# Kernel optimization log

Hardware: AMD Instinct MI355X
Metric: run time of the kernel (lower is better)

The kernel has to match this reference:

```python
import jax, jax.numpy as jnp
import numpy as np
import math

NEG = -10000.0  # module uses -10000, not -inf


def setup_inputs() -> dict:
    key = jax.random.key(0)
    k1, k2, k3 = jax.random.split(key, 3)
    B, Sq, Sk, H, Hkv, D = 2, 2048, 2048, 16, 4, 64
    q = jax.random.normal(k1, (B, Sq, H, D), dtype=jnp.float32)
    kv = jax.random.normal(k2, (B, Sk, 2, Hkv, D), dtype=jnp.float32)
    key_padding_mask = jax.random.randint(k3, (B, Sk), 0, 2) > 0  # True = valid key
    return {"q": q, "kv": kv, "key_padding_mask": key_padding_mask}


def reference(q, kv, key_padding_mask):
    B, Sq, H, D = q.shape
    Sk, Hkv = kv.shape[1], kv.shape[3]
    if Hkv != H:
        # einops repeat '... hkv d -> ... (hkv g) d': each kv head repeated g times contiguously
        kv = jnp.repeat(kv, H // Hkv, axis=3)
    k, v = kv[:, :, 0], kv[:, :, 1]  # [B, Sk, H, D] each
    scale = 1.0 / math.sqrt(D)
    scores = jnp.einsum('bthd,bshd->bhts', q, k * scale)  # [B, H, Sq, Sk]
    # key padding: additive 0 where valid, -10000 where padded
    pad = jnp.where(key_padding_mask, 0.0, NEG).astype(scores.dtype)
    scores = scores + pad[:, None, None, :]
    # causal mask: cols > rows + Sk - Sq gets replaced (not added) with -10000
    rows = jnp.arange(Sq)[:, None]
    cols = jnp.arange(Sk)[None, :]
    causal_mask = cols > rows + (Sk - Sq)
    scores = jnp.where(causal_mask, NEG, scores)
    attention = jax.nn.softmax(scores, axis=-1).astype(v.dtype)
    # dropout p=0.0 -> identity
    output = jnp.einsum('bhts,bshd->bthd', attention, v)  # [B, Sq, H, D]
    return output
```

## Files before the change

### kernel.cpp

```cpp
#include <hip/hip_runtime.h>
#include <math.h>


typedef __bf16 bf16x4 __attribute__((ext_vector_type(4)));
typedef __bf16 bf16x8 __attribute__((ext_vector_type(8)));
typedef float floatx4 __attribute__((ext_vector_type(4)));

#define B_ 2
#define SQ 2048
#define SK 2048
#define H_ 16
#define HKV 4
#define D_ 64
#define QT 64
#define KT 64
#define PADLD 72
#define KVROW 512
#define NEGV (-10000.0f)
#define QSCL 0.18033688f
#define EBIAS 17.3123405f

__global__ __launch_bounds__(256, 4)
void attn_kernel(const float* __restrict__ q,
                 const float* __restrict__ kv,
                 const int* __restrict__ mask,
                 float* __restrict__ out)
{
    __shared__ alignas(16) __bf16 Kt[KT][PADLD];
    __shared__ alignas(16) __bf16 Vt[D_][PADLD];
    __shared__ alignas(16) __bf16 Pl[4][16][PADLD];
    __shared__ float fpart[4][64];
    __shared__ float fw[4][64];
    __shared__ int s_first;

    const int tid  = threadIdx.x;
    const int wave = tid >> 6;
    const int lane = tid & 63;
    const int col  = lane & 15;
    const int quad = lane >> 4;

    if (blockIdx.x < 32) {
        const int bh = (int)blockIdx.x;
        const int b = bh >> 4, h = bh & 15, hkv = h >> 2;
        if (tid == 0) s_first = SK;
        __syncthreads();
        int local = SK;
        for (int s = tid; s < SK; s += 256)
            if (mask[b * SK + s]) local = min(local, s);
        atomicMin(&s_first, local);
        __syncthreads();
        const int nfirst = s_first;
        if (nfirst == 0) return;

        const float* kvb = kv + (size_t)b * SK * KVROW + hkv * D_;
        const float* vvb = kvb + HKV * D_;
        {
            float a0=0,a1=0,a2=0,a3=0,a4=0,a5=0,a6=0,a7=0;
            const int s0 = wave * 512;
            for (int s = s0; s < s0 + 512; s += 8) {
                a0 += vvb[(size_t)(s+0)*KVROW + lane];
                a1 += vvb[(size_t)(s+1)*KVROW + lane];
                a2 += vvb[(size_t)(s+2)*KVROW + lane];
                a3 += vvb[(size_t)(s+3)*KVROW + lane];
                a4 += vvb[(size_t)(s+4)*KVROW + lane];
                a5 += vvb[(size_t)(s+5)*KVROW + lane];
                a6 += vvb[(size_t)(s+6)*KVROW + lane];
                a7 += vvb[(size_t)(s+7)*KVROW + lane];
            }
            fpart[wave][lane] = ((a0+a1)+(a2+a3)) + ((a4+a5)+(a6+a7));
        }
        __syncthreads();
        const float vtotal = fpart[0][lane] + fpart[1][lane]
                           + fpart[2][lane] + fpart[3][lane];

        for (int R = wave; R < nfirst; R += 4) {
            const float* qrow = q + (((size_t)b * SQ + R) * H_ + h) * D_;
            float mymax = -3.4e38f;
            for (int s = lane; s <= R; s += 64) {
                const float* kp = kvb + (size_t)s * KVROW;
                float dt = 0.f;
                for (int d = 0; d < D_; ++d) dt += qrow[d] * kp[d];
                mymax = fmaxf(mymax, dt * 0.125f + NEGV);
            }
#pragma unroll
            for (int off = 32; off >= 1; off >>= 1)
                mymax = fmaxf(mymax, __shfl_xor(mymax, off, 64));
            const float M = (R < SK - 1) ? fmaxf(mymax, NEGV) : mymax;
            float lsum = 0.f, oacc = 0.f, pref = 0.f;
            for (int s0 = 0; s0 <= R; s0 += 64) {
                int s = s0 + lane;
                float w = 0.f;
                if (s <= R) {
                    const float* kp = kvb + (size_t)s * KVROW;
                    float dt = 0.f;
                    for (int d = 0; d < D_; ++d) dt += qrow[d] * kp[d];
                    w = __expf(dt * 0.125f + NEGV - M);
                    lsum += w;
                }
                fw[wave][lane] = w;
                const int nk = (R - s0 + 1 < 64) ? (R - s0 + 1) : 64;
                for (int j = 0; j < nk; ++j) {
                    const float vj = vvb[(size_t)(s0 + j) * KVROW + lane];
                    oacc += fw[wave][j] * vj;
                    pref += vj;
                }
            }
#pragma unroll
            for (int off = 32; off >= 1; off >>= 1)
                lsum += __shfl_xor(lsum, off, 64);
            const float wn   = __expf(NEGV - M);
            const float ltot = lsum + wn * (float)(SK - 1 - R);
            out[(((size_t)b * SQ + R) * H_ + h) * D_ + lane] =
                (oacc + wn * (vtotal - pref)) / ltot;
        }
        return;
    }

    const int id = (int)blockIdx.x - 32;
    const int bh = id & 31;
    const int y  = id >> 5;
    const int kg = y >> 3, jj = y & 7;
    const int qt = (kg == 0) ? 31 - jj : (kg == 1) ? jj : (kg == 2) ? 23 - jj : 8 + jj;
    const int b = bh >> 4, h = bh & 15, hkv = h >> 2;
    const int q0 = qt * QT;
    const int qw = q0 + wave * 16;

    bf16x8 aq[2];
    {
        const int row = qw + col;
        const float* qp = q + (((size_t)b * SQ + row) * H_ + h) * D_ + quad * 8;
#pragma unroll
        for (int kc = 0; kc < 2; ++kc) {
            const float* p = qp + kc * 32;
#pragma unroll
            for (int j = 0; j < 8; ++j) aq[kc][j] = (__bf16)(p[j] * QSCL);
        }
    }

    bf16x8 vone;
#pragma unroll
    for (int j = 0; j < 8; ++j) vone[j] = (__bf16)1.0f;

    floatx4 o[4];
    floatx4 l_acc = (floatx4){0.f, 0.f, 0.f, 0.f};
#pragma unroll
    for (int dj = 0; dj < 4; ++dj) o[dj] = (floatx4){0.f, 0.f, 0.f, 0.f};

    const int kkey = tid >> 4;
    const int kd   = (tid & 15) * 4;
    const int vkey = (tid & 15) * 4;
    const int vd   = (tid >> 4) * 4;

    const float* kvb = kv + (size_t)b * SK * KVROW + hkv * D_;

    float4 kreg[4], vreg[4];
    int mreg = 0;

    auto prefetch = [&](int kt) {
        const float* kb = kvb + (size_t)kt * KT * KVROW;
#pragma unroll
        for (int i = 0; i < 4; ++i)
            kreg[i] = *(const float4*)(kb + (kkey + 16 * i) * KVROW + kd);
        const float* vb = kb + HKV * D_;
#pragma unroll
        for (int i = 0; i < 4; ++i)
            vreg[i] = *(const float4*)(vb + (vkey + i) * KVROW + vd);
        mreg = mask[b * SK + kt * KT + lane];
    };

    auto stage = [&]() {
#pragma unroll
        for (int i = 0; i < 4; ++i) {
            bf16x4 t = { (__bf16)kreg[i].x, (__bf16)kreg[i].y,
                         (__bf16)kreg[i].z, (__bf16)kreg[i].w };
            *(bf16x4*)&Kt[kkey + 16 * i][kd] = t;
        }
        const float* vf = (const float*)vreg;
#pragma unroll
        for (int j = 0; j < 4; ++j) {
            bf16x4 t = { (__bf16)vf[0*4+j], (__bf16)vf[1*4+j],
                         (__bf16)vf[2*4+j], (__bf16)vf[3*4+j] };
            *(bf16x4*)&Vt[vd + j][vkey] = t;
        }
    };

    const int nkt = qt + 1;
    prefetch(0);

    for (int kt = 0; kt < nkt; ++kt) {
        stage();
        const unsigned long long kept = __ballot(mreg != 0);
        __syncthreads();
        if (kt + 1 < nkt) prefetch(kt + 1);

        floatx4 c[4];
#pragma unroll
        for (int kj = 0; kj < 4; ++kj) {
            c[kj] = (floatx4){0.f, 0.f, 0.f, 0.f};
#pragma unroll
            for (int kc = 0; kc < 2; ++kc) {
                bf16x8 bk = *(const bf16x8*)&Kt[kj * 16 + col][kc * 32 + quad * 8];
                c[kj] = __builtin_amdgcn_mfma_f32_16x16x32_bf16(aq[kc], bk, c[kj], 0, 0, 0);
            }
        }
        const bool dg = (kt == qt);
        const int rowl = wave * 16 + quad * 4;
#pragma unroll
        for (int kj = 0; kj < 4; ++kj) {
            const int keyl = kj * 16 + col;
            const bool keep = (kept >> keyl) & 1ull;
#pragma unroll
            for (int r = 0; r < 4; ++r) {
                float p = __builtin_amdgcn_exp2f(c[kj][r] - EBIAS);
                if (!keep) p = 0.f;
                if (dg && keyl > rowl + r) p = 0.f;
                Pl[wave][quad * 4 + r][keyl] = (__bf16)p;
            }
        }
        bf16x8 ap[2];
#pragma unroll
        for (int kc = 0; kc < 2; ++kc)
            ap[kc] = *(const bf16x8*)&Pl[wave][col][kc * 32 + quad * 8];
#pragma unroll
        for (int kc = 0; kc < 2; ++kc)
            l_acc = __builtin_amdgcn_mfma_f32_16x16x32_bf16(ap[kc], vone, l_acc, 0, 0, 0);
#pragma unroll
        for (int dj = 0; dj < 4; ++dj)
#pragma unroll
            for (int kc = 0; kc < 2; ++kc) {
                bf16x8 bv = *(const bf16x8*)&Vt[dj * 16 + col][kc * 32 + quad * 8];
                o[dj] = __builtin_amdgcn_mfma_f32_16x16x32_bf16(ap[kc], bv, o[dj], 0, 0, 0);
            }
        __syncthreads();
    }

#pragma unroll
    for (int r = 0; r < 4; ++r) {
        const float l = l_acc[r];
        if (l > 0.f) {
            const float inv = 1.0f / l;
            const int row = qw + quad * 4 + r;
            float* op = out + (((size_t)b * SQ + row) * H_ + h) * D_ + col;
#pragma unroll
            for (int dj = 0; dj < 4; ++dj)
                op[dj * 16] = o[dj][r] * inv;
        }
    }
}

extern "C" void kernel_launch(void* const* d_in, const int* in_sizes, int n_in,
                              void* d_out, int out_size, void* d_ws, size_t ws_size,
                              hipStream_t stream) {
    const float* q   = (const float*)d_in[0];
    const float* kv  = (const float*)d_in[1];
    const int* mask  = (const int*)d_in[2];
    float* out       = (float*)d_out;
    attn_kernel<<<dim3(32 + 1024), 256, 0, stream>>>(q, kv, mask, out);
}
```

Before: 126.4 us.

## Double query tile to 128 rows per block with two MFMA row groups per wave

Each block now handles 128 query rows, with each wave computing two 16-row groups against every staged K/V tile. This halves the K/V global loads and shared-memory staging per query row, and the grid shrinks to 512 attention blocks. Shared buffers for the fallback path and the main path are overlaid in a union to limit LDS growth, and waves skip tiles lying entirely above the causal diagonal. In exchange it uses more registers (launch bounds lowered to 3), launches fewer blocks so there is less parallelism and coarser load balance, and drops the earlier interleaved tile ordering.

```diff
diff --git a/kernel.cpp b/kernel.cpp
--- a/kernel.cpp
+++ b/kernel.cpp
@@ -12,7 +12,7 @@
 #define H_ 16
 #define HKV 4
 #define D_ 64
-#define QT 64
+#define QT 128
 #define KT 64
 #define PADLD 72
 #define KVROW 512
@@ -20,18 +20,24 @@
 #define QSCL 0.18033688f
 #define EBIAS 17.3123405f
 
-__global__ __launch_bounds__(256, 4)
+__global__ __launch_bounds__(256, 3)
 void attn_kernel(const float* __restrict__ q,
                  const float* __restrict__ kv,
                  const int* __restrict__ mask,
                  float* __restrict__ out)
 {
-    __shared__ alignas(16) __bf16 Kt[KT][PADLD];
-    __shared__ alignas(16) __bf16 Vt[D_][PADLD];
-    __shared__ alignas(16) __bf16 Pl[4][16][PADLD];
-    __shared__ float fpart[4][64];
-    __shared__ float fw[4][64];
-    __shared__ int s_first;
+    __shared__ alignas(16) union {
+        struct {
+            __bf16 Kt[KT][PADLD];
+            __bf16 Vt[D_][PADLD];
+            __bf16 Pl[4][32][PADLD];
+        } m;
+        struct {
+            float fpart[4][64];
+            float fw[4][64];
+            int   s_first;
+        } f;
+    } sh;
 
     const int tid  = threadIdx.x;
     const int wave = tid >> 6;
@@ -42,14 +48,14 @@
     if (blockIdx.x < 32) {
         const int bh = (int)blockIdx.x;
         const int b = bh >> 4, h = bh & 15, hkv = h >> 2;
-        if (tid == 0) s_first = SK;
+        if (tid == 0) sh.f.s_first = SK;
         __syncthreads();
         int local = SK;
         for (int s = tid; s < SK; s += 256)
             if (mask[b * SK + s]) local = min(local, s);
-        atomicMin(&s_first, local);
-        __syncthreads();
-        const int nfirst = s_first;
+        atomicMin(&sh.f.s_first, local);
+        __syncthreads();
+        const int nfirst = sh.f.s_first;
         if (nfirst == 0) return;
 
         const float* kvb = kv + (size_t)b * SK * KVROW + hkv * D_;
@@ -67,11 +73,11 @@
                 a6 += vvb[(size_t)(s+6)*KVROW + lane];
                 a7 += vvb[(size_t)(s+7)*KVROW + lane];
             }
-            fpart[wave][lane] = ((a0+a1)+(a2+a3)) + ((a4+a5)+(a6+a7));
-        }
-        __syncthreads();
-        const float vtotal = fpart[0][lane] + fpart[1][lane]
-                           + fpart[2][lane] + fpart[3][lane];
+            sh.f.fpart[wave][lane] = ((a0+a1)+(a2+a3)) + ((a4+a5)+(a6+a7));
+        }
+        __syncthreads();
+        const float vtotal = sh.f.fpart[0][lane] + sh.f.fpart[1][lane]
+                           + sh.f.fpart[2][lane] + sh.f.fpart[3][lane];
 
         for (int R = wave; R < nfirst; R += 4) {
             const float* qrow = q + (((size_t)b * SQ + R) * H_ + h) * D_;
@@ -97,11 +103,11 @@
                     w = __expf(dt * 0.125f + NEGV - M);
                     lsum += w;
                 }
-                fw[wave][lane] = w;
+                sh.f.fw[wave][lane] = w;
                 const int nk = (R - s0 + 1 < 64) ? (R - s0 + 1) : 64;
                 for (int j = 0; j < nk; ++j) {
                     const float vj = vvb[(size_t)(s0 + j) * KVROW + lane];
-                    oacc += fw[wave][j] * vj;
+                    oacc += sh.f.fw[wave][j] * vj;
                     pref += vj;
                 }
             }
@@ -119,21 +125,21 @@
     const int id = (int)blockIdx.x - 32;
     const int bh = id & 31;
     const int y  = id >> 5;
-    const int kg = y >> 3, jj = y & 7;
-    const int qt = (kg == 0) ? 31 - jj : (kg == 1) ? jj : (kg == 2) ? 23 - jj : 8 + jj;
+    const int qt = 15 - y;
     const int b = bh >> 4, h = bh & 15, hkv = h >> 2;
     const int q0 = qt * QT;
-    const int qw = q0 + wave * 16;
-
-    bf16x8 aq[2];
-    {
-        const int row = qw + col;
+    const int qw = q0 + wave * 32;
+
+    bf16x8 aq[2][2];
+#pragma unroll
+    for (int g = 0; g < 2; ++g) {
+        const int row = qw + g * 16 + col;
         const float* qp = q + (((size_t)b * SQ + row) * H_ + h) * D_ + quad * 8;
 #pragma unroll
         for (int kc = 0; kc < 2; ++kc) {
             const float* p = qp + kc * 32;
 #pragma unroll
-            for (int j = 0; j < 8; ++j) aq[kc][j] = (__bf16)(p[j] * QSCL);
+            for (int j = 0; j < 8; ++j) aq[g][kc][j] = (__bf16)(p[j] * QSCL);
         }
     }
 
@@ -141,10 +147,14 @@
 #pragma unroll
     for (int j = 0; j < 8; ++j) vone[j] = (__bf16)1.0f;
 
-    floatx4 o[4];
-    floatx4 l_acc = (floatx4){0.f, 0.f, 0.f, 0.f};
-#pragma unroll
-    for (int dj = 0; dj < 4; ++dj) o[dj] = (floatx4){0.f, 0.f, 0.f, 0.f};
+    floatx4 o[2][4];
+    floatx4 l_acc[2];
+#pragma unroll
+    for (int g = 0; g < 2; ++g) {
+        l_acc[g] = (floatx4){0.f, 0.f, 0.f, 0.f};
+#pragma unroll
+        for (int dj = 0; dj < 4; ++dj) o[g][dj] = (floatx4){0.f, 0.f, 0.f, 0.f};
+    }
 
     const int kkey = tid >> 4;
     const int kd   = (tid & 15) * 4;
@@ -173,18 +183,18 @@
         for (int i = 0; i < 4; ++i) {
             bf16x4 t = { (__bf16)kreg[i].x, (__bf16)kreg[i].y,
                          (__bf16)kreg[i].z, (__bf16)kreg[i].w };
-            *(bf16x4*)&Kt[kkey + 16 * i][kd] = t;
+            *(bf16x4*)&sh.m.Kt[kkey + 16 * i][kd] = t;
         }
         const float* vf = (const float*)vreg;
 #pragma unroll
         for (int j = 0; j < 4; ++j) {
             bf16x4 t = { (__bf16)vf[0*4+j], (__bf16)vf[1*4+j],
                          (__bf16)vf[2*4+j], (__bf16)vf[3*4+j] };
-            *(bf16x4*)&Vt[vd + j][vkey] = t;
+            *(bf16x4*)&sh.m.Vt[vd + j][vkey] = t;
         }
     };
 
-    const int nkt = qt + 1;
+    const int nkt = 2 * (qt + 1);
     prefetch(0);
 
     for (int kt = 0; kt < nkt; ++kt) {
@@ -193,59 +203,77 @@
         __syncthreads();
         if (kt + 1 < nkt) prefetch(kt + 1);
 
-        floatx4 c[4];
-#pragma unroll
-        for (int kj = 0; kj < 4; ++kj) {
-            c[kj] = (floatx4){0.f, 0.f, 0.f, 0.f};
-#pragma unroll
-            for (int kc = 0; kc < 2; ++kc) {
-                bf16x8 bk = *(const bf16x8*)&Kt[kj * 16 + col][kc * 32 + quad * 8];
-                c[kj] = __builtin_amdgcn_mfma_f32_16x16x32_bf16(aq[kc], bk, c[kj], 0, 0, 0);
-            }
-        }
-        const bool dg = (kt == qt);
-        const int rowl = wave * 16 + quad * 4;
-#pragma unroll
-        for (int kj = 0; kj < 4; ++kj) {
-            const int keyl = kj * 16 + col;
-            const bool keep = (kept >> keyl) & 1ull;
-#pragma unroll
-            for (int r = 0; r < 4; ++r) {
-                float p = __builtin_amdgcn_exp2f(c[kj][r] - EBIAS);
-                if (!keep) p = 0.f;
-                if (dg && keyl > rowl + r) p = 0.f;
-                Pl[wave][quad * 4 + r][keyl] = (__bf16)p;
-            }
-        }
-        bf16x8 ap[2];
-#pragma unroll
-        for (int kc = 0; kc < 2; ++kc)
-            ap[kc] = *(const bf16x8*)&Pl[wave][col][kc * 32 + quad * 8];
-#pragma unroll
-        for (int kc = 0; kc < 2; ++kc)
-            l_acc = __builtin_amdgcn_mfma_f32_16x16x32_bf16(ap[kc], vone, l_acc, 0, 0, 0);
-#pragma unroll
-        for (int dj = 0; dj < 4; ++dj)
-#pragma unroll
-            for (int kc = 0; kc < 2; ++kc) {
-                bf16x8 bv = *(const bf16x8*)&Vt[dj * 16 + col][kc * 32 + quad * 8];
-                o[dj] = __builtin_amdgcn_mfma_f32_16x16x32_bf16(ap[kc], bv, o[dj], 0, 0, 0);
-            }
-        __syncthreads();
-    }
-
-#pragma unroll
-    for (int r = 0; r < 4; ++r) {
-        const float l = l_acc[r];
-        if (l > 0.f) {
-            const float inv = 1.0f / l;
-            const int row = qw + quad * 4 + r;
-            float* op = out + (((size_t)b * SQ + row) * H_ + h) * D_ + col;
+        const int dshift = (2 * qt - kt) * 64;
+        if (dshift + wave * 32 + 31 >= 0) {
+            floatx4 c[2][4];
+#pragma unroll
+            for (int g = 0; g < 2; ++g)
+#pragma unroll
+                for (int kj = 0; kj < 4; ++kj)
+                    c[g][kj] = (floatx4){0.f, 0.f, 0.f, 0.f};
+#pragma unroll
+            for (int kj = 0; kj < 4; ++kj) {
+#pragma unroll
+                for (int kc = 0; kc < 2; ++kc) {
+                    bf16x8 bk = *(const bf16x8*)&sh.m.Kt[kj * 16 + col][kc * 32 + quad * 8];
+                    c[0][kj] = __builtin_amdgcn_mfma_f32_16x16x32_bf16(aq[0][kc], bk, c[0][kj], 0, 0, 0);
+                    c[1][kj] = __builtin_amdgcn_mfma_f32_16x16x32_bf16(aq[1][kc], bk, c[1][kj], 0, 0, 0);
+                }
+            }
+            const bool dg = (dshift < 64);
+#pragma unroll
+            for (int g = 0; g < 2; ++g) {
+                const int rowl = dshift + wave * 32 + g * 16 + quad * 4;
+#pragma unroll
+                for (int kj = 0; kj < 4; ++kj) {
+                    const int keyl = kj * 16 + col;
+                    const bool keep = (kept >> keyl) & 1ull;
+#pragma unroll
+                    for (int r = 0; r < 4; ++r) {
+                        float p = __builtin_amdgcn_exp2f(c[g][kj][r] - EBIAS);
+                        if (!keep) p = 0.f;
+                        if (dg && keyl > rowl + r) p = 0.f;
+                        sh.m.Pl[wave][g * 16 + quad * 4 + r][keyl] = (__bf16)p;
+                    }
+                }
+            }
+            bf16x8 ap[2][2];
+#pragma unroll
+            for (int g = 0; g < 2; ++g)
+#pragma unroll
+                for (int kc = 0; kc < 2; ++kc)
+                    ap[g][kc] = *(const bf16x8*)&sh.m.Pl[wave][g * 16 + col][kc * 32 + quad * 8];
+#pragma unroll
+            for (int g = 0; g < 2; ++g)
+#pragma unroll
+                for (int kc = 0; kc < 2; ++kc)
+                    l_acc[g] = __builtin_amdgcn_mfma_f32_16x16x32_bf16(ap[g][kc], vone, l_acc[g], 0, 0, 0);
 #pragma unroll
             for (int dj = 0; dj < 4; ++dj)
-                op[dj * 16] = o[dj][r] * inv;
-        }
-    }
+#pragma unroll
+                for (int kc = 0; kc < 2; ++kc) {
+                    bf16x8 bv = *(const bf16x8*)&sh.m.Vt[dj * 16 + col][kc * 32 + quad * 8];
+                    o[0][dj] = __builtin_amdgcn_mfma_f32_16x16x32_bf16(ap[0][kc], bv, o[0][dj], 0, 0, 0);
+                    o[1][dj] = __builtin_amdgcn_mfma_f32_16x16x32_bf16(ap[1][kc], bv, o[1][dj], 0, 0, 0);
+                }
+        }
+        __syncthreads();
+    }
+
+#pragma unroll
+    for (int g = 0; g < 2; ++g)
+#pragma unroll
+        for (int r = 0; r < 4; ++r) {
+            const float l = l_acc[g][r];
+            if (l > 0.f) {
+                const float inv = 1.0f / l;
+                const int row = qw + g * 16 + quad * 4 + r;
+                float* op = out + (((size_t)b * SQ + row) * H_ + h) * D_ + col;
+#pragma unroll
+                for (int dj = 0; dj < 4; ++dj)
+                    op[dj * 16] = o[g][dj][r] * inv;
+            }
+        }
 }
 
 extern "C" void kernel_launch(void* const* d_in, const int* in_sizes, int n_in,
@@ -255,5 +283,5 @@
     const float* kv  = (const float*)d_in[1];
     const int* mask  = (const int*)d_in[2];
     float* out       = (float*)d_out;
-    attn_kernel<<<dim3(32 + 1024), 256, 0, stream>>>(q, kv, mask, out);
+    attn_kernel<<<dim3(32 + 512), 256, 0, stream>>>(q, kv, mask, out);
 }
```

Result: slower. 130.1 us (+2.9%).

## Split long causal query tiles across key chunks and combine partials

Applied to the files above, without the earlier changes.

Query tiles with many causal key tiles are now split into up to four chunks of eight key tiles each. Each chunk runs as its own block and writes unnormalized partial outputs and row sums to workspace. A second combine kernel sums the partials and normalizes them. The aim is better load balance and more blocks across the GPU, at the cost of extra workspace traffic and a second launch. The split relies on a fixed softmax bias rather than a per-row running max, so the partial sums can simply be added.

```diff
diff --git a/kernel.cpp b/kernel.cpp
--- a/kernel.cpp
+++ b/kernel.cpp
@@ -19,12 +19,15 @@
 #define NEGV (-10000.0f)
 #define QSCL 0.18033688f
 #define EBIAS 17.3123405f
+#define SLOTF 4160
+#define SLOTS_PER_BH 72
 
 __global__ __launch_bounds__(256, 4)
 void attn_kernel(const float* __restrict__ q,
                  const float* __restrict__ kv,
                  const int* __restrict__ mask,
-                 float* __restrict__ out)
+                 float* __restrict__ out,
+                 float* __restrict__ ws)
 {
     __shared__ alignas(16) __bf16 Kt[KT][PADLD];
     __shared__ alignas(16) __bf16 Vt[D_][PADLD];
@@ -118,9 +121,16 @@
 
     const int id = (int)blockIdx.x - 32;
     const int bh = id & 31;
-    const int y  = id >> 5;
-    const int kg = y >> 3, jj = y & 7;
-    const int qt = (kg == 0) ? 31 - jj : (kg == 1) ? jj : (kg == 2) ? 23 - jj : 8 + jj;
+    const int z  = 79 - (id >> 5);
+    int qt, sp;
+    if (z < 8)       { qt = z;                sp = 0; }
+    else if (z < 24) { qt = 8 + ((z - 8) >> 1);  sp = (z - 8) & 1; }
+    else if (z < 48) { qt = 16 + (z - 24) / 3;   sp = (z - 24) % 3; }
+    else             { qt = 24 + ((z - 48) >> 2); sp = (z - 48) & 3; }
+    const int nsplit = 1 + (qt >> 3);
+    const int k0 = sp * 8;
+    const int k1 = min(qt + 1, k0 + 8);
+
     const int b = bh >> 4, h = bh & 15, hkv = h >> 2;
     const int q0 = qt * QT;
     const int qw = q0 + wave * 16;
@@ -184,14 +194,13 @@
         }
     };
 
-    const int nkt = qt + 1;
-    prefetch(0);
-
-    for (int kt = 0; kt < nkt; ++kt) {
+    prefetch(k0);
+
+    for (int kt = k0; kt < k1; ++kt) {
         stage();
         const unsigned long long kept = __ballot(mreg != 0);
         __syncthreads();
-        if (kt + 1 < nkt) prefetch(kt + 1);
+        if (kt + 1 < k1) prefetch(kt + 1);
 
         floatx4 c[4];
 #pragma unroll
@@ -234,16 +243,71 @@
         __syncthreads();
     }
 
-#pragma unroll
-    for (int r = 0; r < 4; ++r) {
-        const float l = l_acc[r];
-        if (l > 0.f) {
-            const float inv = 1.0f / l;
-            const int row = qw + quad * 4 + r;
-            float* op = out + (((size_t)b * SQ + row) * H_ + h) * D_ + col;
+    if (nsplit == 1) {
+#pragma unroll
+        for (int r = 0; r < 4; ++r) {
+            const float l = l_acc[r];
+            if (l > 0.f) {
+                const float inv = 1.0f / l;
+                const int row = qw + quad * 4 + r;
+                float* op = out + (((size_t)b * SQ + row) * H_ + h) * D_ + col;
+#pragma unroll
+                for (int dj = 0; dj < 4; ++dj)
+                    op[dj * 16] = o[dj][r] * inv;
+            }
+        }
+    } else {
+        const int local0 = (qt < 16) ? (qt - 8) * 2
+                         : (qt < 24) ? 16 + (qt - 16) * 3
+                                     : 40 + (qt - 24) * 4;
+        float* slot = ws + ((size_t)bh * SLOTS_PER_BH + local0 + sp) * SLOTF;
+#pragma unroll
+        for (int r = 0; r < 4; ++r) {
+            const int row = wave * 16 + quad * 4 + r;
+            float* op = slot + (size_t)row * 64 + col;
 #pragma unroll
             for (int dj = 0; dj < 4; ++dj)
-                op[dj * 16] = o[dj][r] * inv;
+                op[dj * 16] = o[dj][r];
+            if (col == 0) slot[4096 + row] = l_acc[r];
+        }
+    }
+}
+
+__global__ __launch_bounds__(256)
+void combine_kernel(const float* __restrict__ ws, float* __restrict__ out)
+{
+    __shared__ float linv[64];
+    const int tid = threadIdx.x;
+    const int bh = (int)blockIdx.x & 31;
+    const int qt = 8 + ((int)blockIdx.x >> 5);
+    const int b = bh >> 4, h = bh & 15;
+    const int n = 1 + (qt >> 3);
+    const int local0 = (qt < 16) ? (qt - 8) * 2
+                     : (qt < 24) ? 16 + (qt - 16) * 3
+                                 : 40 + (qt - 24) * 4;
+    const float* s0 = ws + ((size_t)bh * SLOTS_PER_BH + local0) * SLOTF;
+
+    if (tid < 64) {
+        float s = 0.f;
+        for (int k = 0; k < n; ++k)
+            s += s0[(size_t)k * SLOTF + 4096 + tid];
+        linv[tid] = (s > 0.f) ? 1.0f / s : 0.f;
+    }
+    __syncthreads();
+
+#pragma unroll
+    for (int c = 0; c < 4; ++c) {
+        const int idx = c * 1024 + tid * 4;
+        const int row = idx >> 6, d = idx & 63;
+        float4 acc = *(const float4*)(s0 + idx);
+        for (int k = 1; k < n; ++k) {
+            const float4 t = *(const float4*)(s0 + (size_t)k * SLOTF + idx);
+            acc.x += t.x; acc.y += t.y; acc.z += t.z; acc.w += t.w;
+        }
+        const float inv = linv[row];
+        if (inv > 0.f) {
+            float4 r4 = { acc.x * inv, acc.y * inv, acc.z * inv, acc.w * inv };
+            *(float4*)(out + (((size_t)b * SQ + qt * 64 + row) * H_ + h) * D_ + d) = r4;
         }
     }
 }
@@ -255,5 +319,6 @@
     const float* kv  = (const float*)d_in[1];
     const int* mask  = (const int*)d_in[2];
     float* out       = (float*)d_out;
-    attn_kernel<<<dim3(32 + 1024), 256, 0, stream>>>(q, kv, mask, out);
+    attn_kernel<<<dim3(32 + 2560), 256, 0, stream>>>(q, kv, mask, out, (float*)d_ws);
+    combine_kernel<<<dim3(768), 256, 0, stream>>>((const float*)d_ws, out);
 }
```

Result: slower. 132.0 us (+4.5%).

## Keep softmax probabilities in registers via transposed QK MFMA, drop P LDS roundtrip

Applied to the files above, without the earlier changes.

Computes S^T by swapping the MFMA operands so each lane's accumulator directly matches the A-operand layout of a 16x16x16 bf16 MFMA. The probabilities then feed the PV and row-sum MFMAs from registers instead of being written to and read back from a per-wave shared P tile. Shared memory is also unioned between the fallback path and the main path. The cost is twice as many smaller MFMAs for PV and the row sum, and narrower bf16x4 V loads from LDS.

```diff
diff --git a/kernel.cpp b/kernel.cpp
--- a/kernel.cpp
+++ b/kernel.cpp
@@ -5,6 +5,7 @@
 typedef __bf16 bf16x4 __attribute__((ext_vector_type(4)));
 typedef __bf16 bf16x8 __attribute__((ext_vector_type(8)));
 typedef float floatx4 __attribute__((ext_vector_type(4)));
+typedef short shortx4 __attribute__((ext_vector_type(4)));
 
 #define B_ 2
 #define SQ 2048
@@ -20,18 +21,35 @@
 #define QSCL 0.18033688f
 #define EBIAS 17.3123405f
 
+static __device__ __forceinline__ floatx4 mfma16(bf16x4 a, bf16x4 b, floatx4 c) {
+#if __has_builtin(__builtin_amdgcn_mfma_f32_16x16x16bf16_1k)
+    return __builtin_amdgcn_mfma_f32_16x16x16bf16_1k(
+        __builtin_bit_cast(shortx4, a), __builtin_bit_cast(shortx4, b), c, 0, 0, 0);
+#else
+    floatx4 d;
+    asm("v_mfma_f32_16x16x16_bf16 %0, %1, %2, %3"
+        : "=v"(d) : "v"(a), "v"(b), "v"(c));
+    return d;
+#endif
+}
+
 __global__ __launch_bounds__(256, 4)
 void attn_kernel(const float* __restrict__ q,
                  const float* __restrict__ kv,
                  const int* __restrict__ mask,
                  float* __restrict__ out)
 {
-    __shared__ alignas(16) __bf16 Kt[KT][PADLD];
-    __shared__ alignas(16) __bf16 Vt[D_][PADLD];
-    __shared__ alignas(16) __bf16 Pl[4][16][PADLD];
-    __shared__ float fpart[4][64];
-    __shared__ float fw[4][64];
-    __shared__ int s_first;
+    __shared__ alignas(16) union {
+        struct {
+            __bf16 Kt[KT][PADLD];
+            __bf16 Vt[D_][PADLD];
+        } m;
+        struct {
+            float fpart[4][64];
+            float fw[4][64];
+            int   s_first;
+        } f;
+    } sh;
 
     const int tid  = threadIdx.x;
     const int wave = tid >> 6;
@@ -42,14 +60,14 @@
     if (blockIdx.x < 32) {
         const int bh = (int)blockIdx.x;
         const int b = bh >> 4, h = bh & 15, hkv = h >> 2;
-        if (tid == 0) s_first = SK;
+        if (tid == 0) sh.f.s_first = SK;
         __syncthreads();
         int local = SK;
         for (int s = tid; s < SK; s += 256)
             if (mask[b * SK + s]) local = min(local, s);
-        atomicMin(&s_first, local);
-        __syncthreads();
-        const int nfirst = s_first;
+        atomicMin(&sh.f.s_first, local);
+        __syncthreads();
+        const int nfirst = sh.f.s_first;
         if (nfirst == 0) return;
 
         const float* kvb = kv + (size_t)b * SK * KVROW + hkv * D_;
@@ -67,11 +85,11 @@
                 a6 += vvb[(size_t)(s+6)*KVROW + lane];
                 a7 += vvb[(size_t)(s+7)*KVROW + lane];
             }
-            fpart[wave][lane] = ((a0+a1)+(a2+a3)) + ((a4+a5)+(a6+a7));
-        }
-        __syncthreads();
-        const float vtotal = fpart[0][lane] + fpart[1][lane]
-                           + fpart[2][lane] + fpart[3][lane];
+            sh.f.fpart[wave][lane] = ((a0+a1)+(a2+a3)) + ((a4+a5)+(a6+a7));
+        }
+        __syncthreads();
+        const float vtotal = sh.f.fpart[0][lane] + sh.f.fpart[1][lane]
+                           + sh.f.fpart[2][lane] + sh.f.fpart[3][lane];
 
         for (int R = wave; R < nfirst; R += 4) {
             const float* qrow = q + (((size_t)b * SQ + R) * H_ + h) * D_;
@@ -97,11 +115,11 @@
                     w = __expf(dt * 0.125f + NEGV - M);
                     lsum += w;
                 }
-                fw[wave][lane] = w;
+                sh.f.fw[wave][lane] = w;
                 const int nk = (R - s0 + 1 < 64) ? (R - s0 + 1) : 64;
                 for (int j = 0; j < nk; ++j) {
                     const float vj = vvb[(size_t)(s0 + j) * KVROW + lane];
-                    oacc += fw[wave][j] * vj;
+                    oacc += sh.f.fw[wave][j] * vj;
                     pref += vj;
                 }
             }
@@ -137,9 +155,9 @@
         }
     }
 
-    bf16x8 vone;
-#pragma unroll
-    for (int j = 0; j < 8; ++j) vone[j] = (__bf16)1.0f;
+    bf16x4 vone4;
+#pragma unroll
+    for (int j = 0; j < 4; ++j) vone4[j] = (__bf16)1.0f;
 
     floatx4 o[4];
     floatx4 l_acc = (floatx4){0.f, 0.f, 0.f, 0.f};
@@ -173,14 +191,14 @@
         for (int i = 0; i < 4; ++i) {
             bf16x4 t = { (__bf16)kreg[i].x, (__bf16)kreg[i].y,
                          (__bf16)kreg[i].z, (__bf16)kreg[i].w };
-            *(bf16x4*)&Kt[kkey + 16 * i][kd] = t;
+            *(bf16x4*)&sh.m.Kt[kkey + 16 * i][kd] = t;
         }
         const float* vf = (const float*)vreg;
 #pragma unroll
         for (int j = 0; j < 4; ++j) {
             bf16x4 t = { (__bf16)vf[0*4+j], (__bf16)vf[1*4+j],
                          (__bf16)vf[2*4+j], (__bf16)vf[3*4+j] };
-            *(bf16x4*)&Vt[vd + j][vkey] = t;
+            *(bf16x4*)&sh.m.Vt[vd + j][vkey] = t;
         }
     };
 
@@ -199,37 +217,35 @@
             c[kj] = (floatx4){0.f, 0.f, 0.f, 0.f};
 #pragma unroll
             for (int kc = 0; kc < 2; ++kc) {
-                bf16x8 bk = *(const bf16x8*)&Kt[kj * 16 + col][kc * 32 + quad * 8];
-                c[kj] = __builtin_amdgcn_mfma_f32_16x16x32_bf16(aq[kc], bk, c[kj], 0, 0, 0);
-            }
-        }
+                bf16x8 ak = *(const bf16x8*)&sh.m.Kt[kj * 16 + col][kc * 32 + quad * 8];
+                c[kj] = __builtin_amdgcn_mfma_f32_16x16x32_bf16(ak, aq[kc], c[kj], 0, 0, 0);
+            }
+        }
+
         const bool dg = (kt == qt);
-        const int rowl = wave * 16 + quad * 4;
+        const unsigned long long kq = kept >> (quad * 4);
+        const int tcl = dg ? (wave * 16 + col - quad * 4) : 127;
+        bf16x4 pk[4];
 #pragma unroll
         for (int kj = 0; kj < 4; ++kj) {
-            const int keyl = kj * 16 + col;
-            const bool keep = (kept >> keyl) & 1ull;
 #pragma unroll
             for (int r = 0; r < 4; ++r) {
                 float p = __builtin_amdgcn_exp2f(c[kj][r] - EBIAS);
-                if (!keep) p = 0.f;
-                if (dg && keyl > rowl + r) p = 0.f;
-                Pl[wave][quad * 4 + r][keyl] = (__bf16)p;
-            }
-        }
-        bf16x8 ap[2];
-#pragma unroll
-        for (int kc = 0; kc < 2; ++kc)
-            ap[kc] = *(const bf16x8*)&Pl[wave][col][kc * 32 + quad * 8];
-#pragma unroll
-        for (int kc = 0; kc < 2; ++kc)
-            l_acc = __builtin_amdgcn_mfma_f32_16x16x32_bf16(ap[kc], vone, l_acc, 0, 0, 0);
+                const bool keep = ((kq >> (kj * 16 + r)) & 1ull) && (kj * 16 + r <= tcl);
+                pk[kj][r] = (__bf16)(keep ? p : 0.f);
+            }
+        }
+
+#pragma unroll
+        for (int kj = 0; kj < 4; ++kj)
+            l_acc = mfma16(pk[kj], vone4, l_acc);
+
 #pragma unroll
         for (int dj = 0; dj < 4; ++dj)
 #pragma unroll
-            for (int kc = 0; kc < 2; ++kc) {
-                bf16x8 bv = *(const bf16x8*)&Vt[dj * 16 + col][kc * 32 + quad * 8];
-                o[dj] = __builtin_amdgcn_mfma_f32_16x16x32_bf16(ap[kc], bv, o[dj], 0, 0, 0);
+            for (int kj = 0; kj < 4; ++kj) {
+                bf16x4 bv = *(const bf16x4*)&sh.m.Vt[dj * 16 + col][kj * 16 + quad * 4];
+                o[dj] = mfma16(pk[kj], bv, o[dj]);
             }
         __syncthreads();
     }
```

New measurement: 123.0 us. -2.7%, faster.
